# Performance work log

Measured on AMD Instinct MI355X. Metric: run time of the kernel, lower is better.

## Reference

```python
import jax, jax.numpy as jnp
import numpy as np
import math

T_STEPS = 100      # diffusion steps
TED = 16           # time_embed_dim
NODE_C = 4         # node_num_classes
EDGE_C = 2         # edge_num_classes
HID = 64           # hidden_dim
H = 4              # nhead
B = 256            # graphs per batch
NPG = 64           # nodes per graph
DEG = 8            # avg out-degree
N = B * NPG
E = N * DEG
IN_CH = NODE_C + TED  # 20


def sinusoidal_embedding(t_vec, dim):
    # t_vec: [1] float. Matches get_sinusoidal_embedding for even dim.
    half = dim // 2
    scale = math.log(10000.0) / (half - 1)
    freqs = jnp.exp(-jnp.arange(half, dtype=jnp.float32) * scale)  # [half]
    emb = t_vec[:, None] * freqs[None, :]                          # [1, half]
    return jnp.concatenate([jnp.sin(emb), jnp.cos(emb)], axis=1)   # [1, dim]


def transformer_conv(x, src, dst, Wq, bq, Wk, bk, Wv, bv, Ws, bs):
    # PyG TransformerConv, concat=False (mean over heads), root_weight=True,
    # beta=False, no edge features, dropout=0 (eval).
    n = x.shape[0]
    q = (x @ Wq + bq).reshape(n, H, HID)
    k = (x @ Wk + bk).reshape(n, H, HID)
    v = (x @ Wv + bv).reshape(n, H, HID)
    # attention logits per edge, softmax over incoming edges of each dst node
    logits = jnp.sum(q[dst] * k[src], axis=-1) / math.sqrt(HID)    # [E, H]
    lmax = jax.ops.segment_max(logits, dst, num_segments=n)       # [n, H]
    ex = jnp.exp(logits - lmax[dst])                              # [E, H]
    denom = jax.ops.segment_sum(ex, dst, num_segments=n)          # [n, H]
    attn = ex / jnp.where(denom == 0, 1.0, denom)[dst]            # [E, H]
    msg = v[src] * attn[:, :, None]                               # [E, H, HID]
    agg = jax.ops.segment_sum(msg, dst, num_segments=n)           # [n, H, HID]
    return agg.mean(axis=1) + x @ Ws + bs                         # [n, HID]


def setup_inputs() -> dict:
    key = jax.random.key(0)
    ks = jax.random.split(key, 32)

    # node features: random one-hot labels
    labels = jax.random.randint(ks[0], (N,), 0, NODE_C)
    x = jax.nn.one_hot(labels, NODE_C, dtype=jnp.float32)

    # per-graph random edges (kept within each graph via offsets)
    src_l = jax.random.randint(ks[1], (B, NPG * DEG), 0, NPG)
    dst_l = jax.random.randint(ks[2], (B, NPG * DEG), 0, NPG)
    off = (jnp.arange(B) * NPG)[:, None]
    edge_index = jnp.stack([(src_l + off).reshape(-1), (dst_l + off).reshape(-1)]).astype(jnp.int64)

    batch = jnp.repeat(jnp.arange(B, dtype=jnp.int64), NPG)

    def lin(k, fin, fout):
        kw, kb = jax.random.split(k)
        W = jax.random.normal(kw, (fin, fout), jnp.float32) / math.sqrt(fin)
        b = jax.random.normal(kb, (fout,), jnp.float32) * 0.01
        return W, b

    W_time, b_time = lin(ks[3], TED, TED)
    Wq1, bq1 = lin(ks[4], IN_CH, H * HID)
    Wk1, bk1 = lin(ks[5], IN_CH, H * HID)
    Wv1, bv1 = lin(ks[6], IN_CH, H * HID)
    Ws1, bs1 = lin(ks[7], IN_CH, HID)
    Wq2, bq2 = lin(ks[8], HID, H * HID)
    Wk2, bk2 = lin(ks[9], HID, H * HID)
    Wv2, bv2 = lin(ks[10], HID, H * HID)
    Ws2, bs2 = lin(ks[11], HID, HID)
    W_node, b_node = lin(ks[12], HID, NODE_C)
    W_e1, b_e1 = lin(ks[13], 2 * HID, HID)
    W_e2, b_e2 = lin(ks[14], HID, EDGE_C)

    return dict(x=x, edge_index=edge_index, batch=batch, t=50,
                W_time=W_time, b_time=b_time,
                Wq1=Wq1, bq1=bq1, Wk1=Wk1, bk1=bk1, Wv1=Wv1, bv1=bv1, Ws1=Ws1, bs1=bs1,
                Wq2=Wq2, bq2=bq2, Wk2=Wk2, bk2=bk2, Wv2=Wv2, bv2=bv2, Ws2=Ws2, bs2=bs2,
                W_node=W_node, b_node=b_node, W_e1=W_e1, b_e1=b_e1, W_e2=W_e2, b_e2=b_e2)


def reference(x, edge_index, batch, t,
              W_time, b_time,
              Wq1, bq1, Wk1, bk1, Wv1, bv1, Ws1, bs1,
              Wq2, bq2, Wk2, bk2, Wv2, bv2, Ws2, bs2,
              W_node, b_node, W_e1, b_e1, W_e2, b_e2):
    src, dst = edge_index[0], edge_index[1]

    # time embedding: sinusoidal(t/T) -> Linear -> broadcast to all nodes
    t_vec = jnp.asarray([t], jnp.float32) / T_STEPS
    temb = sinusoidal_embedding(t_vec, TED) @ W_time + b_time      # [1, TED]
    temb = jnp.broadcast_to(temb, (x.shape[0], TED))
    x_in = jnp.concatenate([x, temb], axis=1)                      # [N, 20]

    h = jax.nn.relu(transformer_conv(x_in, src, dst, Wq1, bq1, Wk1, bk1, Wv1, bv1, Ws1, bs1))
    h = jax.nn.relu(transformer_conv(h, src, dst, Wq2, bq2, Wk2, bk2, Wv2, bv2, Ws2, bs2))

    node_logits = h @ W_node + b_node                              # [N, 4]

    # to_dense_batch with equal-sized graphs == reshape; vectorized edge MLP
    hd = h.reshape(B, NPG, HID)
    pair = jnp.concatenate([
        jnp.broadcast_to(hd[:, :, None, :], (B, NPG, NPG, HID)),
        jnp.broadcast_to(hd[:, None, :, :], (B, NPG, NPG, HID)),
    ], axis=-1)                                                    # [B, n, n, 2*HID]
    e_hidden = jax.nn.relu(pair @ W_e1 + b_e1)
    edge_logits = e_hidden @ W_e2 + b_e2                           # [B, n, n, 2]
    return node_logits, edge_logits
```

## Files before the change

kernel.cpp:

```cpp
#include <hip/hip_runtime.h>
#include <math.h>

constexpr int EPG  = 512;
constexpr int ETOT = 131072;

constexpr size_t TAB_Q  = 0;
constexpr size_t TAB_K  = 1024;
constexpr size_t TAB_V  = 2048;
constexpr size_t TAB_S  = 3072;
constexpr size_t TAB_LG = 3328;
constexpr size_t OFF_H2P = 65536;

constexpr int PK_V_HI   = 0;
constexpr int PK_V_LO   = 16384;
constexpr int PK_S_HI   = 32768;
constexpr int PK_S_LO   = 36864;
constexpr int PK_E1T_HI = 40960;
constexpr int PK_E1T_LO = 45056;
constexpr int PK_E1B_HI = 49152;
constexpr int PK_E1B_LO = 53248;
constexpr int PK_M_HI   = 57344;
constexpr int PK_M_LO   = 73728;
constexpr int PK_VV_HI  = 90112;
constexpr int PK_VV_LO  = 91136;
constexpr int PK_N_HI   = 92160;
constexpr int PK_N_LO   = 93184;

typedef short bf16x8 __attribute__((ext_vector_type(8)));
typedef float f32x4  __attribute__((ext_vector_type(4)));

__device__ __forceinline__ short f2bf(float x) {
    unsigned u = __float_as_uint(x);
    u = (u + 0x7fffu + ((u >> 16) & 1u)) >> 16;
    return (short)u;
}
__device__ __forceinline__ float bf2f(short h) {
    return __uint_as_float(((unsigned)(unsigned short)h) << 16);
}
__device__ __forceinline__ void splt(float x, short& hi, short& lo) {
    hi = f2bf(x);
    lo = f2bf(x - bf2f(hi));
}
__device__ __forceinline__ unsigned packsplt(float x) {
    short hi, lo; splt(x, hi, lo);
    return ((unsigned)(unsigned short)hi << 16) | (unsigned short)lo;
}

__device__ __forceinline__ f32x4 mfma3(bf16x8 ah, bf16x8 al, bf16x8 bh, bf16x8 bl, f32x4 c) {
    c = __builtin_amdgcn_mfma_f32_16x16x32_bf16(ah, bh, c, 0, 0, 0);
    c = __builtin_amdgcn_mfma_f32_16x16x32_bf16(ah, bl, c, 0, 0, 0);
    c = __builtin_amdgcn_mfma_f32_16x16x32_bf16(al, bh, c, 0, 0, 0);
    return c;
}

__device__ __forceinline__ bf16x8 ldsfrag(const short* p, int rowb, int kb, int lane) {
    return *(const bf16x8*)&p[(rowb + (lane & 15)) * 72 + kb + ((lane >> 4) << 3)];
}
__device__ __forceinline__ bf16x8 gpfrag(const short* p, int colb, int kb, int lane) {
    return *(const bf16x8*)&p[((colb + (lane & 15)) << 6) + kb + ((lane >> 4) << 3)];
}
__device__ __forceinline__ void unpack8(const unsigned* p, bf16x8& hv, bf16x8& lv) {
    uint4 a = *(const uint4*)p;
    uint4 b = *(const uint4*)(p + 4);
    unsigned u[8] = {a.x, a.y, a.z, a.w, b.x, b.y, b.z, b.w};
    bf16x8 h, l;
    #pragma unroll
    for (int i = 0; i < 8; i++) { h[i] = (short)(u[i] >> 16); l[i] = (short)(u[i] & 0xffffu); }
    hv = h; lv = l;
}

__global__ __launch_bounds__(256) void k_tabprep(
    const int* __restrict__ t_ptr,
    const float* __restrict__ Wt,  const float* __restrict__ bt,
    const float* __restrict__ Wq1, const float* __restrict__ bq1,
    const float* __restrict__ Wk1, const float* __restrict__ bk1,
    const float* __restrict__ Wv1, const float* __restrict__ bv1,
    const float* __restrict__ Ws1, const float* __restrict__ bs1,
    const float* __restrict__ Wq2, const float* __restrict__ bq2,
    const float* __restrict__ Wk2, const float* __restrict__ Wv2,
    const float* __restrict__ Ws2, const float* __restrict__ We1,
    const float* __restrict__ Wn,
    float* __restrict__ ws, short* __restrict__ wsh)
{
    const int t = threadIdx.x, b = blockIdx.x;
    if (b < 112) {
        const float* src; int N; int dhi; int nb;
        if (b < 64)      { src = Wv2;           N = 256; dhi = PK_V_HI;   nb = b; }
        else if (b < 80) { src = Ws2;           N = 64;  dhi = PK_S_HI;   nb = b - 64; }
        else if (b < 96) { src = We1;           N = 64;  dhi = PK_E1T_HI; nb = b - 80; }
        else             { src = We1 + 64 * 64; N = 64;  dhi = PK_E1B_HI; nb = b - 96; }
        int dlo = dhi + N * 64;
        int n = nb * 4 + (t >> 6), kk = t & 63;
        float v = src[(size_t)kk * N + n];
        short hi, lo; splt(v, hi, lo);
        wsh[dhi + n * 64 + kk] = hi;
        wsh[dlo + n * 64 + kk] = lo;
        return;
    }
    if (b < 128) {
        int h = (b - 112) >> 2, m0 = ((b - 112) & 3) * 16;
        __shared__ __align__(16) float wq[64][68];
        __shared__ __align__(16) float wk[16][68];
        for (int i = t; i < 1024; i += 256) {
            int r = i >> 4, c4 = (i & 15) * 4;
            *(float4*)&wq[r][c4] = *(const float4*)&Wq2[(size_t)r * 256 + h * 64 + c4];
        }
        {
            int r = t >> 4, c4 = (t & 15) * 4;
            *(float4*)&wk[r][c4] = *(const float4*)&Wk2[(size_t)(m0 + r) * 256 + h * 64 + c4];
        }
        __syncthreads();
        const int m = m0 + (t >> 4), kk0 = (t & 15) * 4;
        const float* wkr = &wk[t >> 4][0];
        for (int kk = kk0; kk < kk0 + 4; kk++) {
            const float* wqr = &wq[kk][0];
            float acc = 0.f;
            #pragma unroll
            for (int a = 0; a < 64; a += 4) {
                float4 qa = *(const float4*)(wqr + a);
                float4 ka = *(const float4*)(wkr + a);
                acc += qa.x * ka.x + qa.y * ka.y + qa.z * ka.z + qa.w * ka.w;
            }
            acc *= 0.125f;
            short hi, lo; splt(acc, hi, lo);
            wsh[PK_M_HI + h * 4096 + m * 64 + kk] = hi;
            wsh[PK_M_LO + h * 4096 + m * 64 + kk] = lo;
        }
        return;
    }
    if (b < 132) {
        int h = b - 128;
        if (t < 64) {
            float acc = 0.f;
            for (int a = 0; a < 64; a++)
                acc += Wk2[(size_t)t * 256 + h * 64 + a] * bq2[h * 64 + a];
            short hi, lo; splt(0.125f * acc, hi, lo);
            wsh[PK_VV_HI + h * 64 + t] = hi;
            wsh[PK_VV_LO + h * 64 + t] = lo;
        }
        return;
    }
    __shared__ float se[16], temb[16];
    __shared__ float q1t[4][256], k1t[4][256], v1t[4][256], s1t[4][64];
    if (t < 8) {
        float tv = (float)(*t_ptr) * 0.01f;
        float scale = logf(10000.0f) / 7.0f;
        float e = tv * expf(-(float)t * scale);
        se[t]     = sinf(e);
        se[t + 8] = cosf(e);
    }
    __syncthreads();
    if (t < 16) {
        float acc = bt[t];
        for (int i = 0; i < 16; i++) acc += se[i] * Wt[i * 16 + t];
        temb[t] = acc;
    }
    __syncthreads();
    {
        const int o = t;
        float tq = 0.f, tk = 0.f, tv = 0.f;
        for (int d = 0; d < 16; d++) {
            float td = temb[d];
            tq += td * Wq1[(4 + d) * 256 + o];
            tk += td * Wk1[(4 + d) * 256 + o];
            tv += td * Wv1[(4 + d) * 256 + o];
        }
        for (int c = 0; c < 4; c++) {
            q1t[c][o] = Wq1[c * 256 + o] + tq + bq1[o];
            k1t[c][o] = Wk1[c * 256 + o] + tk + bk1[o];
            v1t[c][o] = Wv1[c * 256 + o] + tv + bv1[o];
        }
        if (o < 64) {
            float ts = 0.f;
            for (int d = 0; d < 16; d++) ts += temb[d] * Ws1[(4 + d) * 64 + o];
            for (int c = 0; c < 4; c++) s1t[c][o] = Ws1[c * 64 + o] + ts + bs1[o];
        }
    }
    __syncthreads();
    for (int idx = t; idx < 1024; idx += 256) {
        int c = idx >> 8, o = idx & 255;
        ws[TAB_Q + idx] = q1t[c][o];
        ws[TAB_K + idx] = k1t[c][o];
        ws[TAB_V + idx] = v1t[c][o];
    }
    ws[TAB_S + t] = s1t[t >> 6][t & 63];
    if (t < 64) {
        int cd = t >> 4, cs = (t >> 2) & 3, h = t & 3;
        float acc = 0.f;
        for (int d = 0; d < 64; d++) acc += q1t[cd][h * 64 + d] * k1t[cs][h * 64 + d];
        ws[TAB_LG + t] = acc * 0.125f;
    }
    for (int idx = t; idx < 1024; idx += 256) {
        int c = idx >> 6, k = idx & 63;
        float v = (c < 4) ? Wn[k * 4 + c] : 0.f;
        short hi, lo; splt(v, hi, lo);
        wsh[PK_N_HI + idx] = hi;
        wsh[PK_N_LO + idx] = lo;
    }
    for (int idx = 256 + t; idx < 1024; idx += 256) {
        wsh[PK_VV_HI + idx] = 0;
        wsh[PK_VV_LO + idx] = 0;
    }
}

__global__ __launch_bounds__(512, 4) void k_main(
    const float* __restrict__ x, const int* __restrict__ ei,
    const float* __restrict__ ws, const short* __restrict__ wsh,
    const float* __restrict__ bv, const float* __restrict__ bsk,
    unsigned* __restrict__ h2p)
{
    __shared__ __align__(16) char smem[59008];
    short*    hHi  = (short*)(smem);
    short*    hLo  = (short*)(smem + 9216);
    short*    VtHi = (short*)(smem + 18432);
    short*    VtLo = (short*)(smem + 27648);
    unsigned* Gst  = (unsigned*)(smem + 36864);
    float*    SPf  = (float*)(smem + 45568);
    char*     Cc   = (char*)(smem + 54272);
    float*    wcol = (float*)(smem + 56448);
    float*    lgs  = (float*)(smem + 57472);
    int*      cls  = (int*)(smem + 57728);
    int*      cnt4 = (int*)(smem + 57984);
    float*    v1t  = (float*)(smem + 18432);
    float*    s1t  = (float*)(smem + 22528);

    const int g    = blockIdx.x >> 1;
    const int r0   = (blockIdx.x & 1) * 32;
    const int t    = threadIdx.x;
    const int lane = t & 63, w = t >> 6;
    const int rb   = (w & 1) * 16;
    const int cb   = (w >> 1) * 16;
    const int db   = (w & 3) * 16;
    const int jb0  = (w >> 2) * 32;
    const int lg4  = ((lane >> 4) << 2);
    const int lg8  = ((lane >> 4) << 3);
    const int l15  = lane & 15;
    const int row8 = t >> 3;
    const int d08  = (t & 7) * 8;

    for (int i = t; i < 1024; i += 512) v1t[i] = ws[TAB_V + i];
    if (t < 256) s1t[t] = ws[TAB_S + t];
    if (t < 64)  lgs[t] = ws[TAB_LG + t];
    if (t < 64) {
        const float* xr = x + (size_t)(g * 64 + t) * 4;
        int c = 0;
        if (xr[1] > 0.5f) c = 1;
        if (xr[2] > 0.5f) c = 2;
        if (xr[3] > 0.5f) c = 3;
        cls[t] = c;
    }
    if (t < 256) cnt4[t] = 0;
    for (int i = t; i < 544; i += 512) ((int*)Cc)[i] = 0;
    __syncthreads();

    {
        int ge = g * EPG + t;
        int ls = ei[ge] - g * 64;
        int ld = ei[ETOT + ge] - g * 64;
        atomicAdd(&cnt4[ld * 4 + cls[ls]], 1);
        int lr = ld - r0;
        if ((unsigned)lr < 32u) {
            int idx = lr * 68 + ls;
            atomicAdd((int*)(Cc + (idx & ~3)), 1 << ((idx & 3) * 8));
        }
    }
    __syncthreads();

    {
        int cd = cls[row8];
        int c0 = cnt4[row8 * 4], c1 = cnt4[row8 * 4 + 1],
            c2 = cnt4[row8 * 4 + 2], c3 = cnt4[row8 * 4 + 3];
        float a[16];
        #pragma unroll
        for (int hh = 0; hh < 4; hh++) {
            float l0 = lgs[cd * 16 + hh], l1 = lgs[cd * 16 + 4 + hh],
                  l2 = lgs[cd * 16 + 8 + hh], l3 = lgs[cd * 16 + 12 + hh];
            float m = -1e30f;
            if (c0 > 0) m = fmaxf(m, l0);
            if (c1 > 0) m = fmaxf(m, l1);
            if (c2 > 0) m = fmaxf(m, l2);
            if (c3 > 0) m = fmaxf(m, l3);
            float e0 = (c0 > 0) ? (float)c0 * __expf(l0 - m) : 0.f;
            float e1 = (c1 > 0) ? (float)c1 * __expf(l1 - m) : 0.f;
            float e2 = (c2 > 0) ? (float)c2 * __expf(l2 - m) : 0.f;
            float e3 = (c3 > 0) ? (float)c3 * __expf(l3 - m) : 0.f;
            float den = e0 + e1 + e2 + e3;
            float inv = (den > 0.f) ? 0.25f / den : 0.f;
            a[hh * 4 + 0] = e0 * inv; a[hh * 4 + 1] = e1 * inv;
            a[hh * 4 + 2] = e2 * inv; a[hh * 4 + 3] = e3 * inv;
        }
        bf16x8 vh, vl;
        #pragma unroll
        for (int jj = 0; jj < 8; jj++) {
            int d = d08 + jj;
            float acc = s1t[cd * 64 + d];
            #pragma unroll
            for (int hh = 0; hh < 4; hh++)
                #pragma unroll
                for (int c = 0; c < 4; c++)
                    acc += a[hh * 4 + c] * v1t[c * 256 + hh * 64 + d];
            float o = fmaxf(acc, 0.f);
            short hi, lo; splt(o, hi, lo);
            vh[jj] = hi; vl[jj] = lo;
        }
        *(bf16x8*)&hHi[row8 * 72 + d08] = vh;
        *(bf16x8*)&hLo[row8 * 72 + d08] = vl;
    }
    __syncthreads();

    bf16x8 AhQ0 = ldsfrag(hHi, r0 + rb, 0, lane),  AhQ1 = ldsfrag(hHi, r0 + rb, 32, lane);
    bf16x8 AlQ0 = ldsfrag(hLo, r0 + rb, 0, lane),  AlQ1 = ldsfrag(hLo, r0 + rb, 32, lane);

    f32x4 skacc = {0.f, 0.f, 0.f, 0.f};
    {
        bf16x8 sk0h = gpfrag(wsh + PK_S_HI, cb, 0, lane);
        bf16x8 sk0l = gpfrag(wsh + PK_S_LO, cb, 0, lane);
        bf16x8 sk1h = gpfrag(wsh + PK_S_HI, cb, 32, lane);
        bf16x8 sk1l = gpfrag(wsh + PK_S_LO, cb, 32, lane);
        skacc = mfma3(AhQ0, AlQ0, sk0h, sk0l, skacc);
        skacc = mfma3(AhQ1, AlQ1, sk1h, sk1l, skacc);
        float bb = bsk[cb + l15];
        #pragma unroll
        for (int r = 0; r < 4; r++) skacc[r] += bb;
    }

    if (w < 4) {
        bf16x8 vv0h = gpfrag(wsh + PK_VV_HI, 0, 0, lane);
        bf16x8 vv0l = gpfrag(wsh + PK_VV_LO, 0, 0, lane);
        bf16x8 vv1h = gpfrag(wsh + PK_VV_HI, 0, 32, lane);
        bf16x8 vv1l = gpfrag(wsh + PK_VV_LO, 0, 32, lane);
        bf16x8 a0h = ldsfrag(hHi, w * 16, 0, lane),  a1h = ldsfrag(hHi, w * 16, 32, lane);
        bf16x8 a0l = ldsfrag(hLo, w * 16, 0, lane),  a1l = ldsfrag(hLo, w * 16, 32, lane);
        f32x4 wc = {0.f, 0.f, 0.f, 0.f};
        wc = mfma3(a0h, a0l, vv0h, vv0l, wc);
        wc = mfma3(a1h, a1l, vv1h, vv1l, wc);
        if (l15 < 4) {
            #pragma unroll
            for (int r = 0; r < 4; r++)
                wcol[l15 * 64 + w * 16 + lg4 + r] = wc[r];
        }
    }

    bf16x8 cm0h = gpfrag(wsh + PK_M_HI, cb, 0, lane);
    bf16x8 cm0l = gpfrag(wsh + PK_M_LO, cb, 0, lane);
    bf16x8 cm1h = gpfrag(wsh + PK_M_HI, cb, 32, lane);
    bf16x8 cm1l = gpfrag(wsh + PK_M_LO, cb, 32, lane);
    bf16x8 cv0h = gpfrag(wsh + PK_V_HI, db, 0, lane);
    bf16x8 cv0l = gpfrag(wsh + PK_V_LO, db, 0, lane);
    bf16x8 cv1h = gpfrag(wsh + PK_V_HI, db, 32, lane);
    bf16x8 cv1l = gpfrag(wsh + PK_V_LO, db, 32, lane);
    float4 cbv  = *(const float4*)&bv[db + lg4];

    float hacc[4] = {0.f, 0.f, 0.f, 0.f};
    #pragma unroll 1
    for (int h = 0; h < 4; h++) {
        {
            f32x4 ga = {0.f, 0.f, 0.f, 0.f};
            ga = mfma3(AhQ0, AlQ0, cm0h, cm0l, ga);
            ga = mfma3(AhQ1, AlQ1, cm1h, cm1l, ga);
            #pragma unroll
            for (int r = 0; r < 4; r++)
                Gst[(rb + lg4 + r) * 68 + cb + l15] = packsplt(ga[r]);
        }
        {
            bf16x8 hb00h = ldsfrag(hHi, jb0, 0, lane),       hb00l = ldsfrag(hLo, jb0, 0, lane);
            bf16x8 hb01h = ldsfrag(hHi, jb0, 32, lane),      hb01l = ldsfrag(hLo, jb0, 32, lane);
            bf16x8 hb10h = ldsfrag(hHi, jb0 + 16, 0, lane),  hb10l = ldsfrag(hLo, jb0 + 16, 0, lane);
            bf16x8 hb11h = ldsfrag(hHi, jb0 + 16, 32, lane), hb11l = ldsfrag(hLo, jb0 + 16, 32, lane);
            f32x4 vt0 = {0.f, 0.f, 0.f, 0.f}, vt1 = {0.f, 0.f, 0.f, 0.f};
            vt0 = mfma3(cv0h, cv0l, hb00h, hb00l, vt0);
            vt0 = mfma3(cv1h, cv1l, hb01h, hb01l, vt0);
            vt1 = mfma3(cv0h, cv0l, hb10h, hb10l, vt1);
            vt1 = mfma3(cv1h, cv1l, hb11h, hb11l, vt1);
            #pragma unroll
            for (int r = 0; r < 4; r++) {
                int rr = (db + lg4 + r) * 72;
                short hi, lo;
                splt(vt0[r] + cbv[r], hi, lo);
                VtHi[rr + jb0 + l15] = hi;      VtLo[rr + jb0 + l15] = lo;
                splt(vt1[r] + cbv[r], hi, lo);
                VtHi[rr + jb0 + 16 + l15] = hi; VtLo[rr + jb0 + 16 + l15] = lo;
            }
        }
        __syncthreads();

        int hn = (h + 1) & 3;
        const short* pmh = wsh + PK_M_HI + hn * 4096;
        const short* pml = wsh + PK_M_LO + hn * 4096;
        bf16x8 nm0h = gpfrag(pmh, cb, 0, lane),  nm0l = gpfrag(pml, cb, 0, lane);
        bf16x8 nm1h = gpfrag(pmh, cb, 32, lane), nm1l = gpfrag(pml, cb, 32, lane);
        int gc = hn * 64 + db;
        bf16x8 nv0h = gpfrag(wsh + PK_V_HI, gc, 0, lane);
        bf16x8 nv0l = gpfrag(wsh + PK_V_LO, gc, 0, lane);
        bf16x8 nv1h = gpfrag(wsh + PK_V_HI, gc, 32, lane);
        bf16x8 nv1l = gpfrag(wsh + PK_V_LO, gc, 32, lane);
        float4 nbv  = *(const float4*)&bv[gc + lg4];

        bf16x8 vb0h = ldsfrag(VtHi, cb, 0, lane),  vb0l = ldsfrag(VtLo, cb, 0, lane);
        bf16x8 vb1h = ldsfrag(VtHi, cb, 32, lane), vb1l = ldsfrag(VtLo, cb, 32, lane);
        {
            bf16x8 gh0, gl0, gh1, gl1;
            const unsigned* gp = Gst + (rb + l15) * 68 + lg8;
            unpack8(gp, gh0, gl0);
            unpack8(gp + 32, gh1, gl1);
            bf16x8 sb0h = ldsfrag(hHi, cb, 0, lane),  sb0l = ldsfrag(hLo, cb, 0, lane);
            bf16x8 sb1h = ldsfrag(hHi, cb, 32, lane), sb1l = ldsfrag(hLo, cb, 32, lane);
            f32x4 s = {0.f, 0.f, 0.f, 0.f};
            s = mfma3(gh0, gl0, sb0h, sb0l, s);
            s = mfma3(gh1, gl1, sb1h, sb1l, s);
            #pragma unroll
            for (int r = 0; r < 4; r++)
                SPf[(rb + lg4 + r) * 68 + cb + l15] = s[r];
        }
        __syncthreads();

        {
            const int lr = rb + l15;
            float sv[16];
            {
                const float* sp = SPf + lr * 68;
                float4 a0 = *(const float4*)(sp + lg8);
                float4 a1 = *(const float4*)(sp + lg8 + 4);
                float4 a2 = *(const float4*)(sp + 32 + lg8);
                float4 a3 = *(const float4*)(sp + 32 + lg8 + 4);
                sv[0]=a0.x; sv[1]=a0.y; sv[2]=a0.z; sv[3]=a0.w;
                sv[4]=a1.x; sv[5]=a1.y; sv[6]=a1.z; sv[7]=a1.w;
                sv[8]=a2.x; sv[9]=a2.y; sv[10]=a2.z; sv[11]=a2.w;
                sv[12]=a3.x; sv[13]=a3.y; sv[14]=a3.z; sv[15]=a3.w;
            }
            int cv[16];
            {
                const unsigned* crow = (const unsigned*)(Cc + lr * 68);
                unsigned c0 = crow[lg8 >> 2], c1 = crow[(lg8 >> 2) + 1];
                unsigned c2 = crow[(32 + lg8) >> 2], c3 = crow[((32 + lg8) >> 2) + 1];
                #pragma unroll
                for (int e = 0; e < 4; e++) {
                    cv[e]      = (c0 >> (e * 8)) & 255;
                    cv[4 + e]  = (c1 >> (e * 8)) & 255;
                    cv[8 + e]  = (c2 >> (e * 8)) & 255;
                    cv[12 + e] = (c3 >> (e * 8)) & 255;
                }
            }
            #pragma unroll
            for (int e = 0; e < 8; e++) {
                sv[e]     += wcol[h * 64 + lg8 + e];
                sv[8 + e] += wcol[h * 64 + 32 + lg8 + e];
            }
            float m = -1e30f;
            #pragma unroll
            for (int e = 0; e < 16; e++) if (cv[e] > 0) m = fmaxf(m, sv[e]);
            m = fmaxf(m, __shfl_xor(m, 16));
            m = fmaxf(m, __shfl_xor(m, 32));
            float den = 0.f; float p[16];
            #pragma unroll
            for (int e = 0; e < 16; e++) {
                p[e] = (cv[e] > 0) ? (float)cv[e] * __expf(sv[e] - m) : 0.f;
                den += p[e];
            }
            den += __shfl_xor(den, 16);
            den += __shfl_xor(den, 32);
            float inv = (den > 0.f) ? 1.f / den : 0.f;
            bf16x8 pa0h, pa0l, pa1h, pa1l;
            #pragma unroll
            for (int e = 0; e < 8; e++) {
                short hi, lo;
                splt(p[e] * inv, hi, lo);      pa0h[e] = hi; pa0l[e] = lo;
                splt(p[8 + e] * inv, hi, lo);  pa1h[e] = hi; pa1l[e] = lo;
            }
            f32x4 pv = {0.f, 0.f, 0.f, 0.f};
            pv = mfma3(pa0h, pa0l, vb0h, vb0l, pv);
            pv = mfma3(pa1h, pa1l, vb1h, vb1l, pv);
            #pragma unroll
            for (int r = 0; r < 4; r++) hacc[r] += pv[r];
        }
        cm0h = nm0h; cm0l = nm0l; cm1h = nm1h; cm1l = nm1l;
        cv0h = nv0h; cv0l = nv0l; cv1h = nv1h; cv1l = nv1l;
        cbv = nbv;
    }

    #pragma unroll
    for (int r = 0; r < 4; r++) {
        float v = fmaxf(0.25f * hacc[r] + skacc[r], 0.f);
        h2p[(size_t)(g * 64 + r0 + rb + lg4 + r) * 64 + cb + l15] = packsplt(v);
    }
}

__global__ __launch_bounds__(256) void k_edge(
    const short* __restrict__ wsh, const unsigned* __restrict__ h2g,
    const float* __restrict__ bn, const float* __restrict__ be1,
    const float* __restrict__ We2, const float* __restrict__ be2,
    float* __restrict__ out)
{
    __shared__ __align__(16) char smem[39680];
    unsigned* h2P = (unsigned*)(smem);
    float*    Af  = (float*)(smem + 17408);
    float*    BTf = (float*)(smem + 21760);
    float*    w2s = (float*)(smem + 39168);

    const int g  = blockIdx.x >> 2;
    const int i0 = (blockIdx.x & 3) * 16;
    const int t  = threadIdx.x;
    const int lane = t & 63, w = t >> 6;
    const int lg4 = ((lane >> 4) << 2);
    const int lg8 = ((lane >> 4) << 3);
    const int l15 = lane & 15;

    {
        int row = t >> 2, c16 = (t & 3) * 16;
        const unsigned* src = h2g + (size_t)(g * 64 + row) * 64 + c16;
        #pragma unroll
        for (int q = 0; q < 4; q++)
            *(uint4*)&h2P[row * 68 + c16 + q * 4] = *(const uint4*)(src + q * 4);
    }
    if (t < 128) w2s[(t & 1) * 64 + (t >> 1)] = We2[t];
    __syncthreads();

    {
        bf16x8 aq0, lq0, aq1, lq1;
        const unsigned* ap = h2P + (i0 + l15) * 68;
        unpack8(ap + lg8, aq0, lq0);
        unpack8(ap + 32 + lg8, aq1, lq1);
        {
            int colb = w * 16;
            bf16x8 e0h = gpfrag(wsh + PK_E1T_HI, colb, 0, lane),  e0l = gpfrag(wsh + PK_E1T_LO, colb, 0, lane);
            bf16x8 e1h = gpfrag(wsh + PK_E1T_HI, colb, 32, lane), e1l = gpfrag(wsh + PK_E1T_LO, colb, 32, lane);
            f32x4 aa = {0.f, 0.f, 0.f, 0.f};
            aa = mfma3(aq0, lq0, e0h, e0l, aa);
            aa = mfma3(aq1, lq1, e1h, e1l, aa);
            float bev = be1[colb + l15];
            #pragma unroll
            for (int r = 0; r < 4; r++)
                Af[(lg4 + r) * 68 + colb + l15] = aa[r] + bev;
        }
        if (w == 0) {
            bf16x8 n0h = gpfrag(wsh + PK_N_HI, 0, 0, lane),  n0l = gpfrag(wsh + PK_N_LO, 0, 0, lane);
            bf16x8 n1h = gpfrag(wsh + PK_N_HI, 0, 32, lane), n1l = gpfrag(wsh + PK_N_LO, 0, 32, lane);
            f32x4 nl = {0.f, 0.f, 0.f, 0.f};
            nl = mfma3(aq0, lq0, n0h, n0l, nl);
            nl = mfma3(aq1, lq1, n1h, n1l, nl);
            if (l15 < 4) {
                #pragma unroll
                for (int r = 0; r < 4; r++)
                    out[(size_t)(g * 64 + i0 + lg4 + r) * 4 + l15] = nl[r] + bn[l15];
            }
        }
    }
    {
        bf16x8 af0, lf0, af1, lf1;
        const unsigned* ap = h2P + (w * 16 + l15) * 68;
        unpack8(ap + lg8, af0, lf0);
        unpack8(ap + 32 + lg8, af1, lf1);
        #pragma unroll
        for (int ct = 0; ct < 4; ct++) {
            int colb = ct * 16;
            bf16x8 b0h = gpfrag(wsh + PK_E1B_HI, colb, 0, lane),  b0l = gpfrag(wsh + PK_E1B_LO, colb, 0, lane);
            bf16x8 b1h = gpfrag(wsh + PK_E1B_HI, colb, 32, lane), b1l = gpfrag(wsh + PK_E1B_LO, colb, 32, lane);
            f32x4 bb = {0.f, 0.f, 0.f, 0.f};
            bb = mfma3(af0, lf0, b0h, b0l, bb);
            bb = mfma3(af1, lf1, b1h, b1l, bb);
            #pragma unroll
            for (int r = 0; r < 4; r++)
                BTf[(colb + l15) * 68 + w * 16 + lg4 + r] = bb[r];
        }
    }
    __syncthreads();

    {
        const int j = t & 63;
        float e0[4], e1[4];
        const float cb0 = be2[0], cb1 = be2[1];
        #pragma unroll
        for (int ii = 0; ii < 4; ii++) { e0[ii] = cb0; e1[ii] = cb1; }
        for (int kb = 0; kb < 4; kb++) {
            const int k0 = kb * 16;
            float bj[16], wa[16], wb[16];
            #pragma unroll
            for (int q = 0; q < 16; q++) {
                bj[q] = BTf[(k0 + q) * 68 + j];
                wa[q] = w2s[k0 + q];
                wb[q] = w2s[64 + k0 + q];
            }
            #pragma unroll
            for (int ii = 0; ii < 4; ii++) {
                const float* ar = &Af[(w * 4 + ii) * 68 + k0];
                #pragma unroll
                for (int q = 0; q < 16; q += 4) {
                    float4 a4 = *(const float4*)(ar + q);
                    float s;
                    s = fmaxf(a4.x + bj[q + 0], 0.f); e0[ii] += s * wa[q + 0]; e1[ii] += s * wb[q + 0];
                    s = fmaxf(a4.y + bj[q + 1], 0.f); e0[ii] += s * wa[q + 1]; e1[ii] += s * wb[q + 1];
                    s = fmaxf(a4.z + bj[q + 2], 0.f); e0[ii] += s * wa[q + 2]; e1[ii] += s * wb[q + 2];
                    s = fmaxf(a4.w + bj[q + 3], 0.f); e0[ii] += s * wa[q + 3]; e1[ii] += s * wb[q + 3];
                }
            }
        }
        float2* oe = (float2*)(out + 65536);
        #pragma unroll
        for (int ii = 0; ii < 4; ii++)
            oe[(size_t)(g * 64 + i0 + w * 4 + ii) * 64 + j] = make_float2(e0[ii], e1[ii]);
    }
}

extern "C" void kernel_launch(void* const* d_in, const int* in_sizes, int n_in,
                              void* d_out, int out_size, void* d_ws, size_t ws_size,
                              hipStream_t stream)
{
    const float* x    = (const float*)d_in[0];
    const int*   ei   = (const int*)d_in[1];
    const int*   tptr = (const int*)d_in[3];
    const float* Wt   = (const float*)d_in[4];
    const float* bt   = (const float*)d_in[5];
    const float* Wq1  = (const float*)d_in[6];
    const float* bq1  = (const float*)d_in[7];
    const float* Wk1  = (const float*)d_in[8];
    const float* bk1  = (const float*)d_in[9];
    const float* Wv1  = (const float*)d_in[10];
    const float* bv1  = (const float*)d_in[11];
    const float* Ws1  = (const float*)d_in[12];
    const float* bs1  = (const float*)d_in[13];
    const float* Wq2  = (const float*)d_in[14];
    const float* bq2  = (const float*)d_in[15];
    const float* Wk2  = (const float*)d_in[16];
    const float* Wv2  = (const float*)d_in[18];
    const float* bv2  = (const float*)d_in[19];
    const float* Ws2  = (const float*)d_in[20];
    const float* bs2  = (const float*)d_in[21];
    const float* Wn   = (const float*)d_in[22];
    const float* bn   = (const float*)d_in[23];
    const float* We1  = (const float*)d_in[24];
    const float* be1  = (const float*)d_in[25];
    const float* We2  = (const float*)d_in[26];
    const float* be2  = (const float*)d_in[27];

    float* ws  = (float*)d_ws;
    short* wsh = (short*)(ws + 4096);
    unsigned* h2p = (unsigned*)(ws + OFF_H2P);
    float* out = (float*)d_out;

    k_tabprep<<<133, 256, 0, stream>>>(tptr, Wt, bt, Wq1, bq1, Wk1, bk1, Wv1, bv1,
                                       Ws1, bs1, Wq2, bq2, Wk2, Wv2, Ws2, We1, Wn,
                                       ws, wsh);
    k_main<<<512, 512, 0, stream>>>(x, ei, ws, wsh, bv2, bs2, h2p);
    k_edge<<<1024, 256, 0, stream>>>(wsh, h2p, bn, be1, We2, be2, out);
}
```

Before: 75.57 us.

## Restructure layer-2 kernel to one wave per head over 16-row tiles

The second-layer attention kernel now launches 1024 blocks of 256 threads, each covering 16 destination rows, with each of the 4 waves owning one head. The head loop with per-head block barriers is removed, so each wave runs its own head independently with wave-private LDS scratch. The V projection is reassociated: attention probabilities are multiplied by the transposed layer-1 features first, and then by Wv. Per-head results are summed with a single final barrier. This trades the intra-loop barriers for redundant per-block setup (recomputing h1 for all 64 nodes in four blocks per graph) and more LDS per block (about 77KB), which may lower occupancy.

```diff
diff --git a/kernel.cpp b/kernel.cpp
--- a/kernel.cpp
+++ b/kernel.cpp
@@ -203,43 +203,41 @@
     }
 }
 
-__global__ __launch_bounds__(512, 4) void k_main(
+__global__ __launch_bounds__(256) void k_main(
     const float* __restrict__ x, const int* __restrict__ ei,
     const float* __restrict__ ws, const short* __restrict__ wsh,
     const float* __restrict__ bv, const float* __restrict__ bsk,
     unsigned* __restrict__ h2p)
 {
-    __shared__ __align__(16) char smem[59008];
-    short*    hHi  = (short*)(smem);
-    short*    hLo  = (short*)(smem + 9216);
-    short*    VtHi = (short*)(smem + 18432);
-    short*    VtLo = (short*)(smem + 27648);
-    unsigned* Gst  = (unsigned*)(smem + 36864);
-    float*    SPf  = (float*)(smem + 45568);
-    char*     Cc   = (char*)(smem + 54272);
-    float*    wcol = (float*)(smem + 56448);
-    float*    lgs  = (float*)(smem + 57472);
-    int*      cls  = (int*)(smem + 57728);
-    int*      cnt4 = (int*)(smem + 57984);
-    float*    v1t  = (float*)(smem + 18432);
-    float*    s1t  = (float*)(smem + 22528);
-
-    const int g    = blockIdx.x >> 1;
-    const int r0   = (blockIdx.x & 1) * 32;
+    __shared__ __align__(16) char smem[77376];
+    short* hHi = (short*)(smem);
+    short* hLo = (short*)(smem + 9216);
+    short* tHi = (short*)(smem + 18432);
+    short* tLo = (short*)(smem + 27648);
+    char*  R1base = smem + 36864;
+    char*  R2base = smem + 55296;
+    char*  Cc     = smem + 73728;
+    float* wcolb  = (float*)(smem + 74816);
+    float* lgs    = (float*)(smem + 75840);
+    int*   cls    = (int*)(smem + 76096);
+    int*   cnt4   = (int*)(smem + 76352);
+    float* v1t    = (float*)(smem + 36864);
+    float* s1t    = (float*)(smem + 40960);
+
+    const int g    = blockIdx.x >> 2;
+    const int i0   = (blockIdx.x & 3) * 16;
     const int t    = threadIdx.x;
     const int lane = t & 63, w = t >> 6;
-    const int rb   = (w & 1) * 16;
-    const int cb   = (w >> 1) * 16;
-    const int db   = (w & 3) * 16;
-    const int jb0  = (w >> 2) * 32;
     const int lg4  = ((lane >> 4) << 2);
     const int lg8  = ((lane >> 4) << 3);
     const int l15  = lane & 15;
-    const int row8 = t >> 3;
-    const int d08  = (t & 7) * 8;
-
-    for (int i = t; i < 1024; i += 512) v1t[i] = ws[TAB_V + i];
-    if (t < 256) s1t[t] = ws[TAB_S + t];
+
+    short* GHi = (short*)(R1base + w * 4608);
+    short* GLo = (short*)(R1base + w * 4608 + 2304);
+    float* Sf  = (float*)(R2base + w * 4608);
+
+    for (int i = t; i < 1024; i += 256) v1t[i] = ws[TAB_V + i];
+    s1t[t] = ws[TAB_S + t];
     if (t < 64)  lgs[t] = ws[TAB_LG + t];
     if (t < 64) {
         const float* xr = x + (size_t)(g * 64 + t) * 4;
@@ -249,17 +247,17 @@
         if (xr[3] > 0.5f) c = 3;
         cls[t] = c;
     }
-    if (t < 256) cnt4[t] = 0;
-    for (int i = t; i < 544; i += 512) ((int*)Cc)[i] = 0;
-    __syncthreads();
-
-    {
-        int ge = g * EPG + t;
+    cnt4[t] = 0;
+    for (int i = t; i < 272; i += 256) ((int*)Cc)[i] = 0;
+    __syncthreads();
+
+    for (int e = t; e < EPG; e += 256) {
+        int ge = g * EPG + e;
         int ls = ei[ge] - g * 64;
         int ld = ei[ETOT + ge] - g * 64;
         atomicAdd(&cnt4[ld * 4 + cls[ls]], 1);
-        int lr = ld - r0;
-        if ((unsigned)lr < 32u) {
+        int lr = ld - i0;
+        if ((unsigned)lr < 16u) {
             int idx = lr * 68 + ls;
             atomicAdd((int*)(Cc + (idx & ~3)), 1 << ((idx & 3) * 8));
         }
@@ -267,9 +265,10 @@
     __syncthreads();
 
     {
-        int cd = cls[row8];
-        int c0 = cnt4[row8 * 4], c1 = cnt4[row8 * 4 + 1],
-            c2 = cnt4[row8 * 4 + 2], c3 = cnt4[row8 * 4 + 3];
+        const int row = t >> 2, d0 = (t & 3) * 16;
+        int cd = cls[row];
+        int c0 = cnt4[row * 4], c1 = cnt4[row * 4 + 1],
+            c2 = cnt4[row * 4 + 2], c3 = cnt4[row * 4 + 3];
         float a[16];
         #pragma unroll
         for (int hh = 0; hh < 4; hh++) {
@@ -289,10 +288,10 @@
             a[hh * 4 + 0] = e0 * inv; a[hh * 4 + 1] = e1 * inv;
             a[hh * 4 + 2] = e2 * inv; a[hh * 4 + 3] = e3 * inv;
         }
-        bf16x8 vh, vl;
-        #pragma unroll
-        for (int jj = 0; jj < 8; jj++) {
-            int d = d08 + jj;
+        bf16x8 vh0, vl0, vh1, vl1;
+        #pragma unroll
+        for (int jj = 0; jj < 16; jj++) {
+            int d = d0 + jj;
             float acc = s1t[cd * 64 + d];
             #pragma unroll
             for (int hh = 0; hh < 4; hh++)
@@ -301,187 +300,181 @@
                     acc += a[hh * 4 + c] * v1t[c * 256 + hh * 64 + d];
             float o = fmaxf(acc, 0.f);
             short hi, lo; splt(o, hi, lo);
-            vh[jj] = hi; vl[jj] = lo;
-        }
-        *(bf16x8*)&hHi[row8 * 72 + d08] = vh;
-        *(bf16x8*)&hLo[row8 * 72 + d08] = vl;
-    }
-    __syncthreads();
-
-    bf16x8 AhQ0 = ldsfrag(hHi, r0 + rb, 0, lane),  AhQ1 = ldsfrag(hHi, r0 + rb, 32, lane);
-    bf16x8 AlQ0 = ldsfrag(hLo, r0 + rb, 0, lane),  AlQ1 = ldsfrag(hLo, r0 + rb, 32, lane);
+            if (jj < 8) { vh0[jj] = hi; vl0[jj] = lo; }
+            else        { vh1[jj - 8] = hi; vl1[jj - 8] = lo; }
+            tHi[d * 72 + row] = hi;
+            tLo[d * 72 + row] = lo;
+        }
+        *(bf16x8*)&hHi[row * 72 + d0]     = vh0;
+        *(bf16x8*)&hLo[row * 72 + d0]     = vl0;
+        *(bf16x8*)&hHi[row * 72 + d0 + 8] = vh1;
+        *(bf16x8*)&hLo[row * 72 + d0 + 8] = vl1;
+    }
+    __syncthreads();
+
+    const int h = w;
+
+    bf16x8 AhQ0 = ldsfrag(hHi, i0, 0, lane),  AhQ1 = ldsfrag(hHi, i0, 32, lane);
+    bf16x8 AlQ0 = ldsfrag(hLo, i0, 0, lane),  AlQ1 = ldsfrag(hLo, i0, 32, lane);
 
     f32x4 skacc = {0.f, 0.f, 0.f, 0.f};
     {
-        bf16x8 sk0h = gpfrag(wsh + PK_S_HI, cb, 0, lane);
-        bf16x8 sk0l = gpfrag(wsh + PK_S_LO, cb, 0, lane);
-        bf16x8 sk1h = gpfrag(wsh + PK_S_HI, cb, 32, lane);
-        bf16x8 sk1l = gpfrag(wsh + PK_S_LO, cb, 32, lane);
-        skacc = mfma3(AhQ0, AlQ0, sk0h, sk0l, skacc);
-        skacc = mfma3(AhQ1, AlQ1, sk1h, sk1l, skacc);
+        int cb = w * 16;
+        skacc = mfma3(AhQ0, AlQ0, gpfrag(wsh + PK_S_HI, cb, 0, lane),
+                                   gpfrag(wsh + PK_S_LO, cb, 0, lane), skacc);
+        skacc = mfma3(AhQ1, AlQ1, gpfrag(wsh + PK_S_HI, cb, 32, lane),
+                                   gpfrag(wsh + PK_S_LO, cb, 32, lane), skacc);
         float bb = bsk[cb + l15];
         #pragma unroll
         for (int r = 0; r < 4; r++) skacc[r] += bb;
     }
 
-    if (w < 4) {
+    {
         bf16x8 vv0h = gpfrag(wsh + PK_VV_HI, 0, 0, lane);
         bf16x8 vv0l = gpfrag(wsh + PK_VV_LO, 0, 0, lane);
         bf16x8 vv1h = gpfrag(wsh + PK_VV_HI, 0, 32, lane);
         bf16x8 vv1l = gpfrag(wsh + PK_VV_LO, 0, 32, lane);
-        bf16x8 a0h = ldsfrag(hHi, w * 16, 0, lane),  a1h = ldsfrag(hHi, w * 16, 32, lane);
-        bf16x8 a0l = ldsfrag(hLo, w * 16, 0, lane),  a1l = ldsfrag(hLo, w * 16, 32, lane);
-        f32x4 wc = {0.f, 0.f, 0.f, 0.f};
-        wc = mfma3(a0h, a0l, vv0h, vv0l, wc);
-        wc = mfma3(a1h, a1l, vv1h, vv1l, wc);
-        if (l15 < 4) {
+        #pragma unroll
+        for (int jb = 0; jb < 64; jb += 16) {
+            f32x4 wc = {0.f, 0.f, 0.f, 0.f};
+            wc = mfma3(ldsfrag(hHi, jb, 0, lane),  ldsfrag(hLo, jb, 0, lane),  vv0h, vv0l, wc);
+            wc = mfma3(ldsfrag(hHi, jb, 32, lane), ldsfrag(hLo, jb, 32, lane), vv1h, vv1l, wc);
+            if (l15 == h) {
+                #pragma unroll
+                for (int r = 0; r < 4; r++) wcolb[h * 64 + jb + lg4 + r] = wc[r];
+            }
+        }
+    }
+
+    {
+        const short* pmh = wsh + PK_M_HI + h * 4096;
+        const short* pml = wsh + PK_M_LO + h * 4096;
+        #pragma unroll
+        for (int mb = 0; mb < 64; mb += 16) {
+            f32x4 ga = {0.f, 0.f, 0.f, 0.f};
+            ga = mfma3(AhQ0, AlQ0, gpfrag(pmh, mb, 0, lane),  gpfrag(pml, mb, 0, lane),  ga);
+            ga = mfma3(AhQ1, AlQ1, gpfrag(pmh, mb, 32, lane), gpfrag(pml, mb, 32, lane), ga);
+            #pragma unroll
+            for (int r = 0; r < 4; r++) {
+                short hi, lo; splt(ga[r], hi, lo);
+                GHi[(lg4 + r) * 72 + mb + l15] = hi;
+                GLo[(lg4 + r) * 72 + mb + l15] = lo;
+            }
+        }
+    }
+
+    {
+        bf16x8 g0h = ldsfrag(GHi, 0, 0, lane),  g0l = ldsfrag(GLo, 0, 0, lane);
+        bf16x8 g1h = ldsfrag(GHi, 0, 32, lane), g1l = ldsfrag(GLo, 0, 32, lane);
+        #pragma unroll
+        for (int jb = 0; jb < 64; jb += 16) {
+            f32x4 s = {0.f, 0.f, 0.f, 0.f};
+            s = mfma3(g0h, g0l, ldsfrag(hHi, jb, 0, lane),  ldsfrag(hLo, jb, 0, lane),  s);
+            s = mfma3(g1h, g1l, ldsfrag(hHi, jb, 32, lane), ldsfrag(hLo, jb, 32, lane), s);
             #pragma unroll
             for (int r = 0; r < 4; r++)
-                wcol[l15 * 64 + w * 16 + lg4 + r] = wc[r];
-        }
-    }
-
-    bf16x8 cm0h = gpfrag(wsh + PK_M_HI, cb, 0, lane);
-    bf16x8 cm0l = gpfrag(wsh + PK_M_LO, cb, 0, lane);
-    bf16x8 cm1h = gpfrag(wsh + PK_M_HI, cb, 32, lane);
-    bf16x8 cm1l = gpfrag(wsh + PK_M_LO, cb, 32, lane);
-    bf16x8 cv0h = gpfrag(wsh + PK_V_HI, db, 0, lane);
-    bf16x8 cv0l = gpfrag(wsh + PK_V_LO, db, 0, lane);
-    bf16x8 cv1h = gpfrag(wsh + PK_V_HI, db, 32, lane);
-    bf16x8 cv1l = gpfrag(wsh + PK_V_LO, db, 32, lane);
-    float4 cbv  = *(const float4*)&bv[db + lg4];
-
-    float hacc[4] = {0.f, 0.f, 0.f, 0.f};
-    #pragma unroll 1
-    for (int h = 0; h < 4; h++) {
+                Sf[(lg4 + r) * 68 + jb + l15] = s[r];
+        }
+    }
+
+    bf16x8 pa0h, pa0l, pa1h, pa1l;
+    {
+        const int lr = l15;
+        float sv[16];
         {
-            f32x4 ga = {0.f, 0.f, 0.f, 0.f};
-            ga = mfma3(AhQ0, AlQ0, cm0h, cm0l, ga);
-            ga = mfma3(AhQ1, AlQ1, cm1h, cm1l, ga);
+            const float* sp = Sf + lr * 68;
+            float4 a0 = *(const float4*)(sp + lg8);
+            float4 a1 = *(const float4*)(sp + lg8 + 4);
+            float4 a2 = *(const float4*)(sp + 32 + lg8);
+            float4 a3 = *(const float4*)(sp + 32 + lg8 + 4);
+            sv[0]=a0.x; sv[1]=a0.y; sv[2]=a0.z; sv[3]=a0.w;
+            sv[4]=a1.x; sv[5]=a1.y; sv[6]=a1.z; sv[7]=a1.w;
+            sv[8]=a2.x; sv[9]=a2.y; sv[10]=a2.z; sv[11]=a2.w;
+            sv[12]=a3.x; sv[13]=a3.y; sv[14]=a3.z; sv[15]=a3.w;
+        }
+        int cv[16];
+        {
+            const unsigned* crow = (const unsigned*)(Cc + lr * 68);
+            unsigned c0 = crow[lg8 >> 2], c1 = crow[(lg8 >> 2) + 1];
+            unsigned c2 = crow[(32 + lg8) >> 2], c3 = crow[((32 + lg8) >> 2) + 1];
+            #pragma unroll
+            for (int e = 0; e < 4; e++) {
+                cv[e]      = (c0 >> (e * 8)) & 255;
+                cv[4 + e]  = (c1 >> (e * 8)) & 255;
+                cv[8 + e]  = (c2 >> (e * 8)) & 255;
+                cv[12 + e] = (c3 >> (e * 8)) & 255;
+            }
+        }
+        #pragma unroll
+        for (int e = 0; e < 8; e++) {
+            sv[e]     += wcolb[h * 64 + lg8 + e];
+            sv[8 + e] += wcolb[h * 64 + 32 + lg8 + e];
+        }
+        float m = -1e30f;
+        #pragma unroll
+        for (int e = 0; e < 16; e++) if (cv[e] > 0) m = fmaxf(m, sv[e]);
+        m = fmaxf(m, __shfl_xor(m, 16));
+        m = fmaxf(m, __shfl_xor(m, 32));
+        float den = 0.f; float p[16];
+        #pragma unroll
+        for (int e = 0; e < 16; e++) {
+            p[e] = (cv[e] > 0) ? (float)cv[e] * __expf(sv[e] - m) : 0.f;
+            den += p[e];
+        }
+        den += __shfl_xor(den, 16);
+        den += __shfl_xor(den, 32);
+        float inv = (den > 0.f) ? 1.f / den : 0.f;
+        #pragma unroll
+        for (int e = 0; e < 8; e++) {
+            short hi, lo;
+            splt(p[e] * inv, hi, lo);      pa0h[e] = hi; pa0l[e] = lo;
+            splt(p[8 + e] * inv, hi, lo);  pa1h[e] = hi; pa1l[e] = lo;
+        }
+    }
+
+    #pragma unroll
+    for (int fb = 0; fb < 64; fb += 16) {
+        f32x4 u = {0.f, 0.f, 0.f, 0.f};
+        u = mfma3(pa0h, pa0l, ldsfrag(tHi, fb, 0, lane),  ldsfrag(tLo, fb, 0, lane),  u);
+        u = mfma3(pa1h, pa1l, ldsfrag(tHi, fb, 32, lane), ldsfrag(tLo, fb, 32, lane), u);
+        #pragma unroll
+        for (int r = 0; r < 4; r++) {
+            short hi, lo; splt(u[r], hi, lo);
+            GHi[(lg4 + r) * 72 + fb + l15] = hi;
+            GLo[(lg4 + r) * 72 + fb + l15] = lo;
+        }
+    }
+
+    {
+        bf16x8 u0h = ldsfrag(GHi, 0, 0, lane),  u0l = ldsfrag(GLo, 0, 0, lane);
+        bf16x8 u1h = ldsfrag(GHi, 0, 32, lane), u1l = ldsfrag(GLo, 0, 32, lane);
+        #pragma unroll
+        for (int db = 0; db < 64; db += 16) {
+            int gc = h * 64 + db;
+            f32x4 pv = {0.f, 0.f, 0.f, 0.f};
+            pv = mfma3(u0h, u0l, gpfrag(wsh + PK_V_HI, gc, 0, lane),
+                                  gpfrag(wsh + PK_V_LO, gc, 0, lane), pv);
+            pv = mfma3(u1h, u1l, gpfrag(wsh + PK_V_HI, gc, 32, lane),
+                                  gpfrag(wsh + PK_V_LO, gc, 32, lane), pv);
             #pragma unroll
             for (int r = 0; r < 4; r++)
-                Gst[(rb + lg4 + r) * 68 + cb + l15] = packsplt(ga[r]);
-        }
-        {
-            bf16x8 hb00h = ldsfrag(hHi, jb0, 0, lane),       hb00l = ldsfrag(hLo, jb0, 0, lane);
-            bf16x8 hb01h = ldsfrag(hHi, jb0, 32, lane),      hb01l = ldsfrag(hLo, jb0, 32, lane);
-            bf16x8 hb10h = ldsfrag(hHi, jb0 + 16, 0, lane),  hb10l = ldsfrag(hLo, jb0 + 16, 0, lane);
-            bf16x8 hb11h = ldsfrag(hHi, jb0 + 16, 32, lane), hb11l = ldsfrag(hLo, jb0 + 16, 32, lane);
-            f32x4 vt0 = {0.f, 0.f, 0.f, 0.f}, vt1 = {0.f, 0.f, 0.f, 0.f};
-            vt0 = mfma3(cv0h, cv0l, hb00h, hb00l, vt0);
-            vt0 = mfma3(cv1h, cv1l, hb01h, hb01l, vt0);
-            vt1 = mfma3(cv0h, cv0l, hb10h, hb10l, vt1);
-            vt1 = mfma3(cv1h, cv1l, hb11h, hb11l, vt1);
-            #pragma unroll
-            for (int r = 0; r < 4; r++) {
-                int rr = (db + lg4 + r) * 72;
-                short hi, lo;
-                splt(vt0[r] + cbv[r], hi, lo);
-                VtHi[rr + jb0 + l15] = hi;      VtLo[rr + jb0 + l15] = lo;
-                splt(vt1[r] + cbv[r], hi, lo);
-                VtHi[rr + jb0 + 16 + l15] = hi; VtLo[rr + jb0 + 16 + l15] = lo;
-            }
-        }
-        __syncthreads();
-
-        int hn = (h + 1) & 3;
-        const short* pmh = wsh + PK_M_HI + hn * 4096;
-        const short* pml = wsh + PK_M_LO + hn * 4096;
-        bf16x8 nm0h = gpfrag(pmh, cb, 0, lane),  nm0l = gpfrag(pml, cb, 0, lane);
-        bf16x8 nm1h = gpfrag(pmh, cb, 32, lane), nm1l = gpfrag(pml, cb, 32, lane);
-        int gc = hn * 64 + db;
-        bf16x8 nv0h = gpfrag(wsh + PK_V_HI, gc, 0, lane);
-        bf16x8 nv0l = gpfrag(wsh + PK_V_LO, gc, 0, lane);
-        bf16x8 nv1h = gpfrag(wsh + PK_V_HI, gc, 32, lane);
-        bf16x8 nv1l = gpfrag(wsh + PK_V_LO, gc, 32, lane);
-        float4 nbv  = *(const float4*)&bv[gc + lg4];
-
-        bf16x8 vb0h = ldsfrag(VtHi, cb, 0, lane),  vb0l = ldsfrag(VtLo, cb, 0, lane);
-        bf16x8 vb1h = ldsfrag(VtHi, cb, 32, lane), vb1l = ldsfrag(VtLo, cb, 32, lane);
-        {
-            bf16x8 gh0, gl0, gh1, gl1;
-            const unsigned* gp = Gst + (rb + l15) * 68 + lg8;
-            unpack8(gp, gh0, gl0);
-            unpack8(gp + 32, gh1, gl1);
-            bf16x8 sb0h = ldsfrag(hHi, cb, 0, lane),  sb0l = ldsfrag(hLo, cb, 0, lane);
-            bf16x8 sb1h = ldsfrag(hHi, cb, 32, lane), sb1l = ldsfrag(hLo, cb, 32, lane);
-            f32x4 s = {0.f, 0.f, 0.f, 0.f};
-            s = mfma3(gh0, gl0, sb0h, sb0l, s);
-            s = mfma3(gh1, gl1, sb1h, sb1l, s);
-            #pragma unroll
-            for (int r = 0; r < 4; r++)
-                SPf[(rb + lg4 + r) * 68 + cb + l15] = s[r];
-        }
-        __syncthreads();
-
-        {
-            const int lr = rb + l15;
-            float sv[16];
-            {
-                const float* sp = SPf + lr * 68;
-                float4 a0 = *(const float4*)(sp + lg8);
-                float4 a1 = *(const float4*)(sp + lg8 + 4);
-                float4 a2 = *(const float4*)(sp + 32 + lg8);
-                float4 a3 = *(const float4*)(sp + 32 + lg8 + 4);
-                sv[0]=a0.x; sv[1]=a0.y; sv[2]=a0.z; sv[3]=a0.w;
-                sv[4]=a1.x; sv[5]=a1.y; sv[6]=a1.z; sv[7]=a1.w;
-                sv[8]=a2.x; sv[9]=a2.y; sv[10]=a2.z; sv[11]=a2.w;
-                sv[12]=a3.x; sv[13]=a3.y; sv[14]=a3.z; sv[15]=a3.w;
-            }
-            int cv[16];
-            {
-                const unsigned* crow = (const unsigned*)(Cc + lr * 68);
-                unsigned c0 = crow[lg8 >> 2], c1 = crow[(lg8 >> 2) + 1];
-                unsigned c2 = crow[(32 + lg8) >> 2], c3 = crow[((32 + lg8) >> 2) + 1];
-                #pragma unroll
-                for (int e = 0; e < 4; e++) {
-                    cv[e]      = (c0 >> (e * 8)) & 255;
-                    cv[4 + e]  = (c1 >> (e * 8)) & 255;
-                    cv[8 + e]  = (c2 >> (e * 8)) & 255;
-                    cv[12 + e] = (c3 >> (e * 8)) & 255;
-                }
-            }
-            #pragma unroll
-            for (int e = 0; e < 8; e++) {
-                sv[e]     += wcol[h * 64 + lg8 + e];
-                sv[8 + e] += wcol[h * 64 + 32 + lg8 + e];
-            }
-            float m = -1e30f;
-            #pragma unroll
-            for (int e = 0; e < 16; e++) if (cv[e] > 0) m = fmaxf(m, sv[e]);
-            m = fmaxf(m, __shfl_xor(m, 16));
-            m = fmaxf(m, __shfl_xor(m, 32));
-            float den = 0.f; float p[16];
-            #pragma unroll
-            for (int e = 0; e < 16; e++) {
-                p[e] = (cv[e] > 0) ? (float)cv[e] * __expf(sv[e] - m) : 0.f;
-                den += p[e];
-            }
-            den += __shfl_xor(den, 16);
-            den += __shfl_xor(den, 32);
-            float inv = (den > 0.f) ? 1.f / den : 0.f;
-            bf16x8 pa0h, pa0l, pa1h, pa1l;
-            #pragma unroll
-            for (int e = 0; e < 8; e++) {
-                short hi, lo;
-                splt(p[e] * inv, hi, lo);      pa0h[e] = hi; pa0l[e] = lo;
-                splt(p[8 + e] * inv, hi, lo);  pa1h[e] = hi; pa1l[e] = lo;
-            }
-            f32x4 pv = {0.f, 0.f, 0.f, 0.f};
-            pv = mfma3(pa0h, pa0l, vb0h, vb0l, pv);
-            pv = mfma3(pa1h, pa1l, vb1h, vb1l, pv);
-            #pragma unroll
-            for (int r = 0; r < 4; r++) hacc[r] += pv[r];
-        }
-        cm0h = nm0h; cm0l = nm0l; cm1h = nm1h; cm1l = nm1l;
-        cv0h = nv0h; cv0l = nv0l; cv1h = nv1h; cv1l = nv1l;
-        cbv = nbv;
-    }
-
-    #pragma unroll
-    for (int r = 0; r < 4; r++) {
-        float v = fmaxf(0.25f * hacc[r] + skacc[r], 0.f);
-        h2p[(size_t)(g * 64 + r0 + rb + lg4 + r) * 64 + cb + l15] = packsplt(v);
+                Sf[(lg4 + r) * 68 + db + l15] = pv[r];
+        }
+    }
+    __syncthreads();
+
+    {
+        const int d = w * 16 + l15;
+        float bvsum = bv[d] + bv[64 + d] + bv[128 + d] + bv[192 + d];
+        #pragma unroll
+        for (int r = 0; r < 4; r++) {
+            float sum = 0.f;
+            #pragma unroll
+            for (int hh = 0; hh < 4; hh++)
+                sum += ((const float*)(R2base + hh * 4608))[(lg4 + r) * 68 + d];
+            float v = fmaxf(0.25f * (sum + bvsum) + skacc[r], 0.f);
+            h2p[(size_t)(g * 64 + i0 + lg4 + r) * 64 + d] = packsplt(v);
+        }
     }
 }
 
@@ -640,6 +633,6 @@
     k_tabprep<<<133, 256, 0, stream>>>(tptr, Wt, bt, Wq1, bq1, Wk1, bk1, Wv1, bv1,
                                        Ws1, bs1, Wq2, bq2, Wk2, Wv2, Ws2, We1, Wn,
                                        ws, wsh);
-    k_main<<<512, 512, 0, stream>>>(x, ei, ws, wsh, bv2, bs2, h2p);
+    k_main<<<1024, 256, 0, stream>>>(x, ei, ws, wsh, bv2, bs2, h2p);
     k_edge<<<1024, 256, 0, stream>>>(wsh, h2p, bn, be1, We2, be2, out);
 }
```

Result: faster. 64.02 us (-15.3%).
